# Kernel tuning notes

Hardware: AMD Instinct MI355X
Metric: run time of the kernel (lower is better)

The kernel has to match this reference:

```python
import jax, jax.numpy as jnp
import numpy as np

N_NODES = 100000


def _mean_agg(x, src, dst, n_nodes):
    # gather neighbor (src) features, segment-sum into destination nodes, divide by in-degree
    summed = jax.ops.segment_sum(x[src], dst, num_segments=n_nodes)  # [N, d]
    deg = jax.ops.segment_sum(jnp.ones_like(dst, dtype=x.dtype), dst, num_segments=n_nodes)
    return summed / jnp.clip(deg, 1.0)[:, None]  # DGL clamps zero in-degree to 1


def _sage_conv(x, src, dst, W_self, W_neigh, b, n_nodes):
    h_neigh = _mean_agg(x, src, dst, n_nodes)
    # DGL SAGEConv(mean): fc_self(h_self) + fc_neigh(h_neigh); single bias
    return x @ W_self + h_neigh @ W_neigh + b


def setup_inputs() -> dict:
    key = jax.random.key(0)
    ks = jax.random.split(key, 8)
    in_f, hid_f, out_f = 64, 64, 16
    n_edges = 1200000
    return {
        "x": jax.random.normal(ks[0], (N_NODES, in_f), dtype=jnp.float32),
        "src": jax.random.randint(ks[1], (n_edges,), 0, N_NODES),
        "dst": jax.random.randint(ks[2], (n_edges,), 0, N_NODES),
        "W1_self": jax.random.normal(ks[3], (in_f, hid_f), dtype=jnp.float32) / np.sqrt(in_f),
        "W1_neigh": jax.random.normal(ks[4], (in_f, hid_f), dtype=jnp.float32) / np.sqrt(in_f),
        "b1": jnp.zeros((hid_f,), dtype=jnp.float32),
        "W2_self": jax.random.normal(ks[5], (hid_f, out_f), dtype=jnp.float32) / np.sqrt(hid_f),
        "W2_neigh": jax.random.normal(ks[6], (hid_f, out_f), dtype=jnp.float32) / np.sqrt(hid_f),
        "b2": jnp.zeros((out_f,), dtype=jnp.float32),
    }


def reference(x, src, dst, W1_self, W1_neigh, b1, W2_self, W2_neigh, b2):
    h = _sage_conv(x, src, dst, W1_self, W1_neigh, b1, N_NODES)
    h = jax.nn.relu(h)
    h = _sage_conv(h, src, dst, W2_self, W2_neigh, b2, N_NODES)
    return h
```

## Files before the change

kernel.cpp:

```cpp
#include <hip/hip_runtime.h>

#define N_NODES 100000
#define N_EDGES 1200000
#define NB 391
#define CHUNK_E 4096
#define NBLK_E 293
#define TOT_H (NB * NBLK_E)
#define NSB2 ((TOT_H + 1023) / 1024)

#define OFF_ROWPTR 0
#define OFF_HISTG  400896
#define OFF_HSCAN  859648
#define OFF_BLK2   1318400
#define OFF_PAIRS  1318912
#define OFF_SORTED 6118912
#define OFF_Y1     10918912
#define OFF_H1     23718912

__device__ __forceinline__ unsigned short f2bf(float f) {
    unsigned u = __float_as_uint(f);
    unsigned r = (u + 0x7fffu + ((u >> 16) & 1u)) >> 16;
    return (unsigned short)r;
}


__global__ __launch_bounds__(256) void chunk_hist_kernel(
    const int* __restrict__ dst, int* __restrict__ hist_g)
{
    __shared__ int h[NB];
    const int e0 = blockIdx.x * CHUNK_E;
    const int e1 = min(e0 + CHUNK_E, N_EDGES);
    for (int i = threadIdx.x; i < NB; i += 256) h[i] = 0;
    __syncthreads();
    for (int e = e0 + threadIdx.x; e < e1; e += 256)
        atomicAdd(&h[dst[e] >> 8], 1);
    __syncthreads();
    for (int i = threadIdx.x; i < NB; i += 256)
        hist_g[i * NBLK_E + blockIdx.x] = h[i];
}

__global__ __launch_bounds__(1024) void scan2_blocks_kernel(
    const int* __restrict__ hist_g, int* __restrict__ hs_scan, int* __restrict__ blk2)
{
    __shared__ int s[1024];
    int i = blockIdx.x * 1024 + threadIdx.x;
    int v = (i < TOT_H) ? hist_g[i] : 0;
    s[threadIdx.x] = v;
    __syncthreads();
    for (int off = 1; off < 1024; off <<= 1) {
        int t = (threadIdx.x >= off) ? s[threadIdx.x - off] : 0;
        __syncthreads();
        s[threadIdx.x] += t;
        __syncthreads();
    }
    if (i < TOT_H) hs_scan[i] = s[threadIdx.x] - v;
    if (threadIdx.x == 1023) blk2[blockIdx.x] = s[1023];
}

__global__ __launch_bounds__(128) void scan2_tops_kernel(int* __restrict__ blk2)
{
    __shared__ int s[128];
    int v = (threadIdx.x < NSB2) ? blk2[threadIdx.x] : 0;
    s[threadIdx.x] = v;
    __syncthreads();
    for (int off = 1; off < 128; off <<= 1) {
        int t = (threadIdx.x >= off) ? s[threadIdx.x - off] : 0;
        __syncthreads();
        s[threadIdx.x] += t;
        __syncthreads();
    }
    if (threadIdx.x < NSB2) blk2[threadIdx.x] = s[threadIdx.x] - v;
}

__global__ __launch_bounds__(256) void pair_scatter_kernel(
    const int* __restrict__ src, const int* __restrict__ dst,
    const int* __restrict__ hs_scan, const int* __restrict__ blk2,
    unsigned* __restrict__ pairs)
{
    __shared__ int base_s[NB];
    __shared__ int cur_s[NB];
    const int b = blockIdx.x;
    const int e0 = b * CHUNK_E;
    const int e1 = min(e0 + CHUNK_E, N_EDGES);

    for (int i = threadIdx.x; i < NB; i += 256) {
        int idx = i * NBLK_E + b;
        base_s[i] = hs_scan[idx] + blk2[idx >> 10];
        cur_s[i] = 0;
    }
    __syncthreads();
    for (int e = e0 + threadIdx.x; e < e1; e += 256) {
        int d = dst[e];
        int bk = d >> 8;
        int pos = base_s[bk] + atomicAdd(&cur_s[bk], 1);
        pairs[pos] = ((unsigned)src[e] << 8) | (unsigned)(d & 255);
    }
}

__global__ __launch_bounds__(256) void bucket_fill_plus_kernel(
    const unsigned* __restrict__ pairs,
    const int* __restrict__ hs_scan, const int* __restrict__ blk2,
    int* __restrict__ row_ptr, int* __restrict__ sorted_src)
{
    __shared__ int hist[256];
    __shared__ int sc[256];
    __shared__ int cur[256];
    const int b = blockIdx.x;
    const int t = threadIdx.x;

    int i0 = b * NBLK_E;
    const int start = hs_scan[i0] + blk2[i0 >> 10];
    int end;
    if (b == NB - 1) end = N_EDGES;
    else {
        int i1 = (b + 1) * NBLK_E;
        end = hs_scan[i1] + blk2[i1 >> 10];
    }

    hist[t] = 0;
    __syncthreads();
    for (int e = start + t; e < end; e += 256)
        atomicAdd(&hist[pairs[e] & 255u], 1);
    __syncthreads();

    int v = hist[t];
    sc[t] = v;
    __syncthreads();
    for (int off = 1; off < 256; off <<= 1) {
        int tv = (t >= off) ? sc[t - off] : 0;
        __syncthreads();
        sc[t] += tv;
        __syncthreads();
    }
    const int excl = sc[t] - v;
    const int node = (b << 8) + t;
    if (node < N_NODES) row_ptr[node] = start + excl;
    if (b == NB - 1 && t == 0) row_ptr[N_NODES] = N_EDGES;
    cur[t] = start + excl;
    __syncthreads();

    for (int e = start + t; e < end; e += 256) {
        unsigned u = pairs[e];
        int pos = atomicAdd(&cur[u & 255u], 1);
        sorted_src[pos] = (int)(u >> 8);
    }
}


__global__ __launch_bounds__(256) void dense1_kernel(
    const float* __restrict__ x,
    const float* __restrict__ Wn, const float* __restrict__ Ws,
    const float* __restrict__ b,
    unsigned short* __restrict__ y1, float* __restrict__ z1)
{
    __shared__ float sx[32 * 64];
    const int t = threadIdx.x;
    const int w = t >> 6;
    const int lane = t & 63;
    const int half = w >> 1;
    const int nsub = (w & 1) * 16;
    const int chunk = blockIdx.x * 32;

    {
        const float4* gx = (const float4*)(x + (size_t)chunk * 64);
        float4* sx4 = (float4*)sx;
        sx4[t] = gx[t];
        sx4[t + 256] = gx[t + 256];
    }

    const float* W = half ? Ws : Wn;
    float wr[64];
#pragma unroll
    for (int k = 0; k < 64; ++k) wr[k] = W[k * 64 + lane];
    const float bj = half ? b[lane] : 0.f;

    __syncthreads();

#pragma unroll 1
    for (int m = 0; m < 16; ++m) {
        const int node = nsub + m;
        const float4* xr = (const float4*)(sx + node * 64);
        float a0 = 0.f, a1 = 0.f, a2 = 0.f, a3 = 0.f;
#pragma unroll
        for (int k4 = 0; k4 < 16; ++k4) {
            float4 v = xr[k4];
            a0 += v.x * wr[4 * k4 + 0];
            a1 += v.y * wr[4 * k4 + 1];
            a2 += v.z * wr[4 * k4 + 2];
            a3 += v.w * wr[4 * k4 + 3];
        }
        const float o = (a0 + a1) + (a2 + a3) + bj;
        const size_t gn = (size_t)(chunk + node);
        if (half) z1[gn * 64 + lane] = o;
        else      y1[gn * 64 + lane] = f2bf(o);
    }
}

__global__ __launch_bounds__(256) void dense2_kernel(
    const float* __restrict__ h1,
    const float* __restrict__ Wn, const float* __restrict__ Ws,
    const float* __restrict__ b,
    float* __restrict__ y2, float* __restrict__ out)
{
    __shared__ float sx[32 * 68];
    const int t = threadIdx.x;
    const int w = t >> 6;
    const int lane = t & 63;
    const int half = w >> 1;
    const int nsub = (w & 1) * 16;
    const int j = lane & 15;
    const int g = lane >> 4;
    const int chunk = blockIdx.x * 32;

    {
        const float4* gx = (const float4*)(h1 + (size_t)chunk * 64);
        float4* sx4 = (float4*)sx;
        int r0 = t >> 4, c0 = t & 15;
        sx4[r0 * 17 + c0] = gx[t];
        sx4[(r0 + 16) * 17 + c0] = gx[t + 256];
    }

    const float* W = half ? Ws : Wn;
    float wr[64];
#pragma unroll
    for (int k = 0; k < 64; ++k) wr[k] = W[k * 16 + j];
    const float bj = half ? b[j] : 0.f;

    __syncthreads();

#pragma unroll 1
    for (int q = 0; q < 4; ++q) {
        const int node = nsub + q * 4 + g;
        const float4* xr = (const float4*)(sx + node * 68);
        float a0 = 0.f, a1 = 0.f, a2 = 0.f, a3 = 0.f;
#pragma unroll
        for (int k4 = 0; k4 < 16; ++k4) {
            float4 v = xr[k4];
            a0 += v.x * wr[4 * k4 + 0];
            a1 += v.y * wr[4 * k4 + 1];
            a2 += v.z * wr[4 * k4 + 2];
            a3 += v.w * wr[4 * k4 + 3];
        }
        const float o = (a0 + a1) + (a2 + a3) + bj;
        const size_t gn = (size_t)(chunk + node);
        if (half) out[gn * 16 + j] = o;
        else      y2[gn * 16 + j] = o;
    }
}


__global__ __launch_bounds__(256) void gather1_kernel(
    const unsigned short* __restrict__ y1,
    const int* __restrict__ row_ptr,
    const int* __restrict__ sorted_src,
    float* __restrict__ h1)
{
    const int w = threadIdx.x >> 6;
    const int lane = threadIdx.x & 63;
    const int n = blockIdx.x * 4 + w;
    const int g = lane >> 3;
    const int fl = lane & 7;

    const int start = row_ptr[n];
    const int deg = row_ptr[n + 1] - start;

    float a0 = 0.f, a1 = 0.f, a2 = 0.f, a3 = 0.f;
    float a4 = 0.f, a5 = 0.f, a6 = 0.f, a7 = 0.f;
    for (int base = 0; base < deg; base += 64) {
        const int m = min(64, deg - base);
        int eid = 0;
        if (lane < m) eid = sorted_src[start + base + lane];
        for (int jj = 0; jj < m; jj += 8) {
            const int idx = jj + g;
            const int s = __shfl(eid, idx);
            if (idx < m) {
                uint4 raw = ((const uint4*)(y1 + (size_t)s * 64))[fl];
                a0 += __uint_as_float(raw.x << 16);
                a1 += __uint_as_float(raw.x & 0xffff0000u);
                a2 += __uint_as_float(raw.y << 16);
                a3 += __uint_as_float(raw.y & 0xffff0000u);
                a4 += __uint_as_float(raw.z << 16);
                a5 += __uint_as_float(raw.z & 0xffff0000u);
                a6 += __uint_as_float(raw.w << 16);
                a7 += __uint_as_float(raw.w & 0xffff0000u);
            }
        }
    }
#pragma unroll
    for (int d = 8; d <= 32; d <<= 1) {
        a0 += __shfl_xor(a0, d); a1 += __shfl_xor(a1, d);
        a2 += __shfl_xor(a2, d); a3 += __shfl_xor(a3, d);
        a4 += __shfl_xor(a4, d); a5 += __shfl_xor(a5, d);
        a6 += __shfl_xor(a6, d); a7 += __shfl_xor(a7, d);
    }

    const float invd = 1.0f / (float)max(deg, 1);
    if (g == 0) {
        float4* hp = (float4*)(h1 + (size_t)n * 64);
        float4 z0 = hp[fl * 2];
        float4 z1v = hp[fl * 2 + 1];
        hp[fl * 2] = make_float4(fmaxf(z0.x + a0 * invd, 0.f),
                                 fmaxf(z0.y + a1 * invd, 0.f),
                                 fmaxf(z0.z + a2 * invd, 0.f),
                                 fmaxf(z0.w + a3 * invd, 0.f));
        hp[fl * 2 + 1] = make_float4(fmaxf(z1v.x + a4 * invd, 0.f),
                                     fmaxf(z1v.y + a5 * invd, 0.f),
                                     fmaxf(z1v.z + a6 * invd, 0.f),
                                     fmaxf(z1v.w + a7 * invd, 0.f));
    }
}

__global__ __launch_bounds__(256) void gather2_kernel(
    const float* __restrict__ y2,
    const int* __restrict__ row_ptr,
    const int* __restrict__ sorted_src,
    float* __restrict__ out)
{
    const int w = threadIdx.x >> 6;
    const int lane = threadIdx.x & 63;
    const int n = blockIdx.x * 4 + w;
    const int group = lane >> 2;
    const int fl = lane & 3;

    const int start = row_ptr[n];
    const int deg = row_ptr[n + 1] - start;

    float4 acc = make_float4(0.f, 0.f, 0.f, 0.f);
    for (int base = 0; base < deg; base += 64) {
        const int m = min(64, deg - base);
        int eid = 0;
        if (lane < m) eid = sorted_src[start + base + lane];
        for (int jj = 0; jj < m; jj += 16) {
            const int idx = jj + group;
            const int s = __shfl(eid, idx);
            if (idx < m) {
                float4 v = ((const float4*)(y2 + (size_t)s * 16))[fl];
                acc.x += v.x; acc.y += v.y; acc.z += v.z; acc.w += v.w;
            }
        }
    }
#pragma unroll
    for (int d = 4; d <= 32; d <<= 1) {
        acc.x += __shfl_xor(acc.x, d); acc.y += __shfl_xor(acc.y, d);
        acc.z += __shfl_xor(acc.z, d); acc.w += __shfl_xor(acc.w, d);
    }
    const float invd = 1.0f / (float)max(deg, 1);
    if (lane < 4) {
        float4* op = (float4*)(out + (size_t)n * 16);
        float4 z = op[fl];
        op[fl] = make_float4(z.x + acc.x * invd, z.y + acc.y * invd,
                             z.z + acc.z * invd, z.w + acc.w * invd);
    }
}

extern "C" void kernel_launch(void* const* d_in, const int* in_sizes, int n_in,
                              void* d_out, int out_size, void* d_ws, size_t ws_size,
                              hipStream_t stream) {
    const float* x   = (const float*)d_in[0];
    const int*   src = (const int*)d_in[1];
    const int*   dst = (const int*)d_in[2];
    const float* W1s = (const float*)d_in[3];
    const float* W1n = (const float*)d_in[4];
    const float* b1  = (const float*)d_in[5];
    const float* W2s = (const float*)d_in[6];
    const float* W2n = (const float*)d_in[7];
    const float* b2  = (const float*)d_in[8];
    float* out = (float*)d_out;

    char* ws = (char*)d_ws;
    int* row_ptr    = (int*)(ws + OFF_ROWPTR);
    int* hist_g     = (int*)(ws + OFF_HISTG);
    int* hs_scan    = (int*)(ws + OFF_HSCAN);
    int* blk2       = (int*)(ws + OFF_BLK2);
    unsigned* pairs = (unsigned*)(ws + OFF_PAIRS);
    int* sorted_src = (int*)(ws + OFF_SORTED);
    unsigned short* y1 = (unsigned short*)(ws + OFF_Y1);
    float* y2       = (float*)(ws + OFF_Y1);
    float* h1       = (float*)(ws + OFF_H1);

    chunk_hist_kernel<<<NBLK_E, 256, 0, stream>>>(dst, hist_g);
    scan2_blocks_kernel<<<NSB2, 1024, 0, stream>>>(hist_g, hs_scan, blk2);
    scan2_tops_kernel<<<1, 128, 0, stream>>>(blk2);
    pair_scatter_kernel<<<NBLK_E, 256, 0, stream>>>(src, dst, hs_scan, blk2, pairs);
    bucket_fill_plus_kernel<<<NB, 256, 0, stream>>>(pairs, hs_scan, blk2, row_ptr, sorted_src);

    dense1_kernel<<<3125, 256, 0, stream>>>(x, W1n, W1s, b1, y1, h1);
    gather1_kernel<<<N_NODES / 4, 256, 0, stream>>>(y1, row_ptr, sorted_src, h1);

    dense2_kernel<<<3125, 256, 0, stream>>>(h1, W2n, W2s, b2, y2, out);
    gather2_kernel<<<N_NODES / 4, 256, 0, stream>>>(y2, row_ptr, sorted_src, out);
}
```

Baseline: 245.8 us.

## Fuse bucket fill into layer-1 gather with shared-memory neighbor lists

Drops the separate bucket_fill kernel and does the per-bucket counting sort inside the first gather kernel. Buckets shrink from 256 to 128 nodes, so each block's edge list (about 1536 edges) fits in a 4096-entry shared array. Layer 1 then reads neighbor ids from LDS, and sorted_src and row_ptr are still written out for layer 2. The cost is only 782 blocks of 512 threads, each wave walking 16 nodes in series, which lowers the parallelism available to hide gather latency compared with one wave per node.

```diff
diff --git a/kernel.cpp b/kernel.cpp
--- a/kernel.cpp
+++ b/kernel.cpp
@@ -2,20 +2,22 @@
 
 #define N_NODES 100000
 #define N_EDGES 1200000
-#define NB 391
+#define BK 128
+#define NB 782
 #define CHUNK_E 4096
 #define NBLK_E 293
 #define TOT_H (NB * NBLK_E)
 #define NSB2 ((TOT_H + 1023) / 1024)
+#define CAP 4096
 
 #define OFF_ROWPTR 0
 #define OFF_HISTG  400896
-#define OFF_HSCAN  859648
-#define OFF_BLK2   1318400
-#define OFF_PAIRS  1318912
-#define OFF_SORTED 6118912
-#define OFF_Y1     10918912
-#define OFF_H1     23718912
+#define OFF_HSCAN  1317632
+#define OFF_BLK2   2234368
+#define OFF_PAIRS  2235392
+#define OFF_SORTED 7035392
+#define OFF_Y1     11835392
+#define OFF_H1     24635392
 
 __device__ __forceinline__ unsigned short f2bf(float f) {
     unsigned u = __float_as_uint(f);
@@ -33,7 +35,7 @@
     for (int i = threadIdx.x; i < NB; i += 256) h[i] = 0;
     __syncthreads();
     for (int e = e0 + threadIdx.x; e < e1; e += 256)
-        atomicAdd(&h[dst[e] >> 8], 1);
+        atomicAdd(&h[dst[e] >> 7], 1);
     __syncthreads();
     for (int i = threadIdx.x; i < NB; i += 256)
         hist_g[i * NBLK_E + blockIdx.x] = h[i];
@@ -57,13 +59,13 @@
     if (threadIdx.x == 1023) blk2[blockIdx.x] = s[1023];
 }
 
-__global__ __launch_bounds__(128) void scan2_tops_kernel(int* __restrict__ blk2)
-{
-    __shared__ int s[128];
+__global__ __launch_bounds__(256) void scan2_tops_kernel(int* __restrict__ blk2)
+{
+    __shared__ int s[256];
     int v = (threadIdx.x < NSB2) ? blk2[threadIdx.x] : 0;
     s[threadIdx.x] = v;
     __syncthreads();
-    for (int off = 1; off < 128; off <<= 1) {
+    for (int off = 1; off < 256; off <<= 1) {
         int t = (threadIdx.x >= off) ? s[threadIdx.x - off] : 0;
         __syncthreads();
         s[threadIdx.x] += t;
@@ -91,58 +93,9 @@
     __syncthreads();
     for (int e = e0 + threadIdx.x; e < e1; e += 256) {
         int d = dst[e];
-        int bk = d >> 8;
+        int bk = d >> 7;
         int pos = base_s[bk] + atomicAdd(&cur_s[bk], 1);
-        pairs[pos] = ((unsigned)src[e] << 8) | (unsigned)(d & 255);
-    }
-}
-
-__global__ __launch_bounds__(256) void bucket_fill_plus_kernel(
-    const unsigned* __restrict__ pairs,
-    const int* __restrict__ hs_scan, const int* __restrict__ blk2,
-    int* __restrict__ row_ptr, int* __restrict__ sorted_src)
-{
-    __shared__ int hist[256];
-    __shared__ int sc[256];
-    __shared__ int cur[256];
-    const int b = blockIdx.x;
-    const int t = threadIdx.x;
-
-    int i0 = b * NBLK_E;
-    const int start = hs_scan[i0] + blk2[i0 >> 10];
-    int end;
-    if (b == NB - 1) end = N_EDGES;
-    else {
-        int i1 = (b + 1) * NBLK_E;
-        end = hs_scan[i1] + blk2[i1 >> 10];
-    }
-
-    hist[t] = 0;
-    __syncthreads();
-    for (int e = start + t; e < end; e += 256)
-        atomicAdd(&hist[pairs[e] & 255u], 1);
-    __syncthreads();
-
-    int v = hist[t];
-    sc[t] = v;
-    __syncthreads();
-    for (int off = 1; off < 256; off <<= 1) {
-        int tv = (t >= off) ? sc[t - off] : 0;
-        __syncthreads();
-        sc[t] += tv;
-        __syncthreads();
-    }
-    const int excl = sc[t] - v;
-    const int node = (b << 8) + t;
-    if (node < N_NODES) row_ptr[node] = start + excl;
-    if (b == NB - 1 && t == 0) row_ptr[N_NODES] = N_EDGES;
-    cur[t] = start + excl;
-    __syncthreads();
-
-    for (int e = start + t; e < end; e += 256) {
-        unsigned u = pairs[e];
-        int pos = atomicAdd(&cur[u & 255u], 1);
-        sorted_src[pos] = (int)(u >> 8);
+        pairs[pos] = ((unsigned)src[e] << 7) | (unsigned)(d & 127);
     }
 }
 
@@ -248,65 +201,160 @@
     }
 }
 
-
-__global__ __launch_bounds__(256) void gather1_kernel(
+__global__ __launch_bounds__(512) void fused_gather1_kernel(
     const unsigned short* __restrict__ y1,
-    const int* __restrict__ row_ptr,
-    const int* __restrict__ sorted_src,
+    const unsigned* __restrict__ pairs,
+    const int* __restrict__ hs_scan, const int* __restrict__ blk2,
+    int* __restrict__ row_ptr, int* __restrict__ sorted_src,
     float* __restrict__ h1)
 {
-    const int w = threadIdx.x >> 6;
-    const int lane = threadIdx.x & 63;
-    const int n = blockIdx.x * 4 + w;
+    __shared__ int slist[CAP];
+    __shared__ int hist[BK];
+    __shared__ int sc[BK];
+    __shared__ int cur[BK];
+    const int b = blockIdx.x;
+    const int t = threadIdx.x;
+    const int lane = t & 63;
+    const int wv = t >> 6;
     const int g = lane >> 3;
     const int fl = lane & 7;
 
-    const int start = row_ptr[n];
-    const int deg = row_ptr[n + 1] - start;
-
-    float a0 = 0.f, a1 = 0.f, a2 = 0.f, a3 = 0.f;
-    float a4 = 0.f, a5 = 0.f, a6 = 0.f, a7 = 0.f;
-    for (int base = 0; base < deg; base += 64) {
-        const int m = min(64, deg - base);
-        int eid = 0;
-        if (lane < m) eid = sorted_src[start + base + lane];
-        for (int jj = 0; jj < m; jj += 8) {
-            const int idx = jj + g;
-            const int s = __shfl(eid, idx);
-            if (idx < m) {
-                uint4 raw = ((const uint4*)(y1 + (size_t)s * 64))[fl];
-                a0 += __uint_as_float(raw.x << 16);
-                a1 += __uint_as_float(raw.x & 0xffff0000u);
-                a2 += __uint_as_float(raw.y << 16);
-                a3 += __uint_as_float(raw.y & 0xffff0000u);
-                a4 += __uint_as_float(raw.z << 16);
-                a5 += __uint_as_float(raw.z & 0xffff0000u);
-                a6 += __uint_as_float(raw.w << 16);
-                a7 += __uint_as_float(raw.w & 0xffff0000u);
-            }
-        }
-    }
-#pragma unroll
-    for (int d = 8; d <= 32; d <<= 1) {
-        a0 += __shfl_xor(a0, d); a1 += __shfl_xor(a1, d);
-        a2 += __shfl_xor(a2, d); a3 += __shfl_xor(a3, d);
-        a4 += __shfl_xor(a4, d); a5 += __shfl_xor(a5, d);
-        a6 += __shfl_xor(a6, d); a7 += __shfl_xor(a7, d);
-    }
-
-    const float invd = 1.0f / (float)max(deg, 1);
-    if (g == 0) {
-        float4* hp = (float4*)(h1 + (size_t)n * 64);
-        float4 z0 = hp[fl * 2];
-        float4 z1v = hp[fl * 2 + 1];
-        hp[fl * 2] = make_float4(fmaxf(z0.x + a0 * invd, 0.f),
-                                 fmaxf(z0.y + a1 * invd, 0.f),
-                                 fmaxf(z0.z + a2 * invd, 0.f),
-                                 fmaxf(z0.w + a3 * invd, 0.f));
-        hp[fl * 2 + 1] = make_float4(fmaxf(z1v.x + a4 * invd, 0.f),
-                                     fmaxf(z1v.y + a5 * invd, 0.f),
-                                     fmaxf(z1v.z + a6 * invd, 0.f),
-                                     fmaxf(z1v.w + a7 * invd, 0.f));
+    const int i0 = b * NBLK_E;
+    const int start = hs_scan[i0] + blk2[i0 >> 10];
+    const int end = (b == NB - 1) ? N_EDGES
+                    : hs_scan[i0 + NBLK_E] + blk2[(i0 + NBLK_E) >> 10];
+    const int cnt = end - start;
+    const int node0 = b * BK;
+
+    if (t < BK) hist[t] = 0;
+    __syncthreads();
+    for (int e = start + t; e < end; e += 512)
+        atomicAdd(&hist[pairs[e] & 127u], 1);
+    __syncthreads();
+
+    int v = (t < BK) ? hist[t] : 0;
+    if (t < BK) sc[t] = v;
+    __syncthreads();
+    for (int off = 1; off < BK; off <<= 1) {
+        int tv = (t >= off && t < BK) ? sc[t - off] : 0;
+        __syncthreads();
+        if (t < BK) sc[t] += tv;
+        __syncthreads();
+    }
+    const int excl = (t < BK) ? sc[t] - v : 0;
+    if (t < BK && node0 + t < N_NODES) row_ptr[node0 + t] = start + excl;
+    if (b == NB - 1 && t == 0) row_ptr[N_NODES] = N_EDGES;
+    if (t < BK) cur[t] = excl;
+    __syncthreads();
+
+    if (cnt <= CAP) {
+        for (int e = start + t; e < end; e += 512) {
+            unsigned u = pairs[e];
+            int p = atomicAdd(&cur[u & 127u], 1);
+            slist[p] = (int)(u >> 7);
+        }
+        __syncthreads();
+        for (int i = t; i < cnt; i += 512)
+            sorted_src[start + i] = slist[i];
+        for (int m = 0; m < 16; ++m) {
+            const int node = wv * 16 + m;
+            const int gn = node0 + node;
+            if (gn >= N_NODES) break;
+            const int o = sc[node] - hist[node];
+            const int dg = hist[node];
+            float a0 = 0.f, a1 = 0.f, a2 = 0.f, a3 = 0.f;
+            float a4 = 0.f, a5 = 0.f, a6 = 0.f, a7 = 0.f;
+            for (int base = 0; base < dg; base += 8) {
+                const int idx = base + g;
+                if (idx < dg) {
+                    const int s = slist[o + idx];
+                    uint4 raw = ((const uint4*)(y1 + (size_t)s * 64))[fl];
+                    a0 += __uint_as_float(raw.x << 16);
+                    a1 += __uint_as_float(raw.x & 0xffff0000u);
+                    a2 += __uint_as_float(raw.y << 16);
+                    a3 += __uint_as_float(raw.y & 0xffff0000u);
+                    a4 += __uint_as_float(raw.z << 16);
+                    a5 += __uint_as_float(raw.z & 0xffff0000u);
+                    a6 += __uint_as_float(raw.w << 16);
+                    a7 += __uint_as_float(raw.w & 0xffff0000u);
+                }
+            }
+#pragma unroll
+            for (int d = 8; d <= 32; d <<= 1) {
+                a0 += __shfl_xor(a0, d); a1 += __shfl_xor(a1, d);
+                a2 += __shfl_xor(a2, d); a3 += __shfl_xor(a3, d);
+                a4 += __shfl_xor(a4, d); a5 += __shfl_xor(a5, d);
+                a6 += __shfl_xor(a6, d); a7 += __shfl_xor(a7, d);
+            }
+            const float invd = 1.0f / (float)max(dg, 1);
+            if (g == 0) {
+                float4* hp = (float4*)(h1 + (size_t)gn * 64);
+                float4 z0 = hp[fl * 2];
+                float4 z1v = hp[fl * 2 + 1];
+                hp[fl * 2] = make_float4(fmaxf(z0.x + a0 * invd, 0.f),
+                                         fmaxf(z0.y + a1 * invd, 0.f),
+                                         fmaxf(z0.z + a2 * invd, 0.f),
+                                         fmaxf(z0.w + a3 * invd, 0.f));
+                hp[fl * 2 + 1] = make_float4(fmaxf(z1v.x + a4 * invd, 0.f),
+                                             fmaxf(z1v.y + a5 * invd, 0.f),
+                                             fmaxf(z1v.z + a6 * invd, 0.f),
+                                             fmaxf(z1v.w + a7 * invd, 0.f));
+            }
+        }
+    } else {
+        if (t < BK) cur[t] = start + excl;
+        __syncthreads();
+        for (int e = start + t; e < end; e += 512) {
+            unsigned u = pairs[e];
+            int p = atomicAdd(&cur[u & 127u], 1);
+            sorted_src[p] = (int)(u >> 7);
+        }
+        __syncthreads();
+        for (int m = 0; m < 16; ++m) {
+            const int node = wv * 16 + m;
+            const int gn = node0 + node;
+            if (gn >= N_NODES) break;
+            const int o = start + sc[node] - hist[node];
+            const int dg = hist[node];
+            float a0 = 0.f, a1 = 0.f, a2 = 0.f, a3 = 0.f;
+            float a4 = 0.f, a5 = 0.f, a6 = 0.f, a7 = 0.f;
+            for (int base = 0; base < dg; base += 8) {
+                const int idx = base + g;
+                if (idx < dg) {
+                    const int s = sorted_src[o + idx];
+                    uint4 raw = ((const uint4*)(y1 + (size_t)s * 64))[fl];
+                    a0 += __uint_as_float(raw.x << 16);
+                    a1 += __uint_as_float(raw.x & 0xffff0000u);
+                    a2 += __uint_as_float(raw.y << 16);
+                    a3 += __uint_as_float(raw.y & 0xffff0000u);
+                    a4 += __uint_as_float(raw.z << 16);
+                    a5 += __uint_as_float(raw.z & 0xffff0000u);
+                    a6 += __uint_as_float(raw.w << 16);
+                    a7 += __uint_as_float(raw.w & 0xffff0000u);
+                }
+            }
+#pragma unroll
+            for (int d = 8; d <= 32; d <<= 1) {
+                a0 += __shfl_xor(a0, d); a1 += __shfl_xor(a1, d);
+                a2 += __shfl_xor(a2, d); a3 += __shfl_xor(a3, d);
+                a4 += __shfl_xor(a4, d); a5 += __shfl_xor(a5, d);
+                a6 += __shfl_xor(a6, d); a7 += __shfl_xor(a7, d);
+            }
+            const float invd = 1.0f / (float)max(dg, 1);
+            if (g == 0) {
+                float4* hp = (float4*)(h1 + (size_t)gn * 64);
+                float4 z0 = hp[fl * 2];
+                float4 z1v = hp[fl * 2 + 1];
+                hp[fl * 2] = make_float4(fmaxf(z0.x + a0 * invd, 0.f),
+                                         fmaxf(z0.y + a1 * invd, 0.f),
+                                         fmaxf(z0.z + a2 * invd, 0.f),
+                                         fmaxf(z0.w + a3 * invd, 0.f));
+                hp[fl * 2 + 1] = make_float4(fmaxf(z1v.x + a4 * invd, 0.f),
+                                             fmaxf(z1v.y + a5 * invd, 0.f),
+                                             fmaxf(z1v.z + a6 * invd, 0.f),
+                                             fmaxf(z1v.w + a7 * invd, 0.f));
+            }
+        }
     }
 }
 
@@ -380,12 +428,12 @@
 
     chunk_hist_kernel<<<NBLK_E, 256, 0, stream>>>(dst, hist_g);
     scan2_blocks_kernel<<<NSB2, 1024, 0, stream>>>(hist_g, hs_scan, blk2);
-    scan2_tops_kernel<<<1, 128, 0, stream>>>(blk2);
+    scan2_tops_kernel<<<1, 256, 0, stream>>>(blk2);
     pair_scatter_kernel<<<NBLK_E, 256, 0, stream>>>(src, dst, hs_scan, blk2, pairs);
-    bucket_fill_plus_kernel<<<NB, 256, 0, stream>>>(pairs, hs_scan, blk2, row_ptr, sorted_src);
 
     dense1_kernel<<<3125, 256, 0, stream>>>(x, W1n, W1s, b1, y1, h1);
-    gather1_kernel<<<N_NODES / 4, 256, 0, stream>>>(y1, row_ptr, sorted_src, h1);
+    fused_gather1_kernel<<<NB, 512, 0, stream>>>(y1, pairs, hs_scan, blk2,
+                                                 row_ptr, sorted_src, h1);
 
     dense2_kernel<<<3125, 256, 0, stream>>>(h1, W2n, W2s, b2, y2, out);
     gather2_kernel<<<N_NODES / 4, 256, 0, stream>>>(y2, row_ptr, sorted_src, out);
```

New measurement: 247.4 us. Within noise of the previous version (+0.7%).
